# Kernel optimization log

Measured on AMD Instinct MI355X. Metric: run time of the kernel, lower is better.

Reference implementation:

```python
import jax, jax.numpy as jnp
import numpy as np

N = 100_000        # nodes
E_HALF = 1_600_000 # undirected edges; symmetrized -> 3.2M directed
N_IN, N_HEMB, N_HGCN, N_OUT = 128, 32, 32, 1


def setup_inputs() -> dict:
    key = jax.random.key(0)
    ks = jax.random.split(key, 8)
    x = jax.random.normal(ks[0], (N, N_IN), dtype=jnp.float32)
    t = jax.random.uniform(ks[1], (N,), dtype=jnp.float32)
    # symmetric edge list (A = A^T), matching the typical undirected-graph usage
    src = jax.random.randint(ks[2], (E_HALF,), 0, N)
    dst = jax.random.randint(ks[3], (E_HALF,), 0, N)
    row = jnp.concatenate([src, dst]).astype(jnp.int32)
    col = jnp.concatenate([dst, src]).astype(jnp.int32)
    s = 0.05
    W_emb = jax.random.normal(ks[4], (N_IN, N_HEMB), jnp.float32) * s
    b_emb = jnp.zeros((N_HEMB,), jnp.float32)
    W_gcn = jax.random.normal(ks[5], (N_HEMB, N_HGCN), jnp.float32) * s
    b_gcn = jnp.zeros((N_HGCN,), jnp.float32)
    W1 = jax.random.normal(ks[6], (N_HGCN + 2, N_HEMB), jnp.float32) * s
    b1 = jnp.zeros((N_HEMB,), jnp.float32)
    W2 = jax.random.normal(ks[7], (N_HEMB, N_OUT), jnp.float32) * s
    b2 = jnp.zeros((N_OUT,), jnp.float32)
    return dict(x=x, t=t, row=row, col=col,
                W_emb=W_emb, b_emb=b_emb, W_gcn=W_gcn, b_gcn=b_gcn,
                W1=W1, b1=b1, W2=W2, b2=b2)


def reference(x, t, row, col, W_emb, b_emb, W_gcn, b_gcn, W1, b1, W2, b2):
    n = x.shape[0]
    h = jax.nn.relu(x @ W_emb + b_emb)                        # [N, Hemb]
    # per-edge attention score via gather + dot
    att = jnp.einsum('eh,eh->e', h[row], h[col])              # [E]
    att = jnp.exp(att - att.max())                            # global-max stabilized exp
    # per-node softmax denominator (segment sum over neighbors) + eps
    deno = jax.ops.segment_sum(att, row, num_segments=n) + 1e-8
    att = att / deno[row]                                     # normalized edge attention
    # exposure z: attention-weighted neighbor treatments
    z = jax.ops.segment_sum(att * t[col], row, num_segments=n)  # [N]
    # GCNConv (unit edge values: set_value() is non-inplace so adj_t stays valueless;
    # PyG then fills 1s, adds self loops, symmetric D^-1/2 norm)
    deg = jax.ops.segment_sum(jnp.ones(row.shape, jnp.float32), col, num_segments=n) + 1.0
    dis = jax.lax.rsqrt(deg)                                  # [N], deg >= 1
    hw = h @ W_gcn                                            # [N, Hgcn]
    msg = dis[row][:, None] * hw[row]                         # [E, Hgcn]
    agg = jax.ops.segment_sum(msg, col, num_segments=n)       # [N, Hgcn]
    gcn = dis[:, None] * agg + (dis * dis)[:, None] * hw + b_gcn
    rep = h + jax.nn.relu(gcn)                                # residual node rep
    feats = jnp.concatenate([rep, t[:, None], z[:, None]], axis=1)  # [N, Hgcn+2]
    out = jax.nn.relu(feats @ W1 + b1) @ W2 + b2              # [N, 1]
    return out, rep, z
```

## Files before the change

### kernel.cpp

```cpp
#include <hip/hip_runtime.h>
#include <hip/hip_bf16.h>
#include <hip/hip_fp16.h>

static constexpr int HN = 32;
static constexpr int NIN = 128;
static constexpr int CH1 = 8192;
static constexpr int CAP2 = 12288;
static constexpr float SQRT_LOG2E = 1.2011224087864498f;

typedef _Float16 h2v __attribute__((ext_vector_type(2)));

__device__ __forceinline__ float bf2f(unsigned short u) {
    union { unsigned int i; float f; } v;
    v.i = ((unsigned int)u) << 16;
    return v.f;
}
__device__ __forceinline__ float ldf(const void* p, size_t i, int isbf) {
    return isbf ? bf2f(((const unsigned short*)p)[i]) : ((const float*)p)[i];
}
__device__ __forceinline__ unsigned int pack2h(float a, float b) {
    unsigned short ua = __half_as_ushort(__float2half_rn(a));
    unsigned short ub = __half_as_ushort(__float2half_rn(b));
    return (unsigned int)ua | ((unsigned int)ub << 16);
}
__device__ __forceinline__ float2 up2(unsigned int u) {
    __half2 h2;
    *reinterpret_cast<unsigned int*>(&h2) = u;
    return __half22float2(h2);
}
__device__ __forceinline__ float fd2(unsigned int a, unsigned int b, float c) {
#if __has_builtin(__builtin_amdgcn_fdot2)
    return __builtin_amdgcn_fdot2(__builtin_bit_cast(h2v, a),
                                  __builtin_bit_cast(h2v, b), c, false);
#else
    float2 fa = up2(a), fb = up2(b);
    return c + fa.x * fb.x + fa.y * fb.y;
#endif
}
__device__ __forceinline__ unsigned int fmap(float f) {
    unsigned int u = __float_as_uint(f);
    return (f >= 0.f) ? (u | 0x80000000u) : ~u;
}
__device__ __forceinline__ float funmap(unsigned int u) {
    return (u & 0x80000000u) ? __uint_as_float(u & 0x7FFFFFFFu)
                             : __uint_as_float(~u);
}

__global__ __launch_bounds__(256) void embed1_kernel(
    const void* __restrict__ x,
    const void* __restrict__ Wemb,
    const void* __restrict__ bemb,
    const int* __restrict__ flagp,
    float* __restrict__ h, int N)
{
    __shared__ float We[NIN * HN];
    __shared__ float be[HN];
    __shared__ float xs[32][NIN];
    const int tid = threadIdx.x;
    const int isbf = flagp[0];

    for (int i = tid; i < NIN * HN; i += 256) We[i] = ldf(Wemb, i, isbf);
    if (tid < HN) be[tid] = ldf(bemb, tid, isbf);

    const int n0 = blockIdx.x * 32;
    if (isbf) {
        const ushort4* x4 = (const ushort4*)((const unsigned short*)x + (size_t)n0 * NIN);
        for (int i = tid; i < 32 * (NIN / 4); i += 256) {
            ushort4 u = x4[i];
            int base = i * 4, n = base >> 7, k = base & (NIN - 1);
            xs[n][k] = bf2f(u.x); xs[n][k + 1] = bf2f(u.y);
            xs[n][k + 2] = bf2f(u.z); xs[n][k + 3] = bf2f(u.w);
        }
    } else {
        const float4* x4 = (const float4*)((const float*)x + (size_t)n0 * NIN);
        for (int i = tid; i < 32 * (NIN / 4); i += 256) {
            float4 u = x4[i];
            int base = i * 4, n = base >> 7, k = base & (NIN - 1);
            xs[n][k] = u.x; xs[n][k + 1] = u.y;
            xs[n][k + 2] = u.z; xs[n][k + 3] = u.w;
        }
    }
    __syncthreads();

    const int f = tid & 31, ns = tid >> 5;
    float a0 = be[f], a1 = be[f], a2 = be[f], a3 = be[f];
    #pragma unroll 8
    for (int k = 0; k < NIN; ++k) {
        float w = We[k * HN + f];
        a0 += xs[ns +  0][k] * w;
        a1 += xs[ns +  8][k] * w;
        a2 += xs[ns + 16][k] * w;
        a3 += xs[ns + 24][k] * w;
    }
    if (n0 + ns      < N) h[(size_t)(n0 + ns     ) * HN + f] = fmaxf(a0, 0.f);
    if (n0 + ns +  8 < N) h[(size_t)(n0 + ns +  8) * HN + f] = fmaxf(a1, 0.f);
    if (n0 + ns + 16 < N) h[(size_t)(n0 + ns + 16) * HN + f] = fmaxf(a2, 0.f);
    if (n0 + ns + 24 < N) h[(size_t)(n0 + ns + 24) * HN + f] = fmaxf(a3, 0.f);
}

__global__ __launch_bounds__(512) void bhist_kernel(
    const int* __restrict__ col, int* __restrict__ bucket_cnt, int E, int B,
    int* __restrict__ blkhist,
    const unsigned int* __restrict__ xw, int* __restrict__ flag)
{
    __shared__ int hist[512];
    const int t = threadIdx.x;
    const int e0 = blockIdx.x * CH1;
    for (int i = t; i < B; i += 512) hist[i] = 0;
    if (blockIdx.x == 0 && t < 64) {
        int hits = 0;
        #pragma unroll
        for (int k = 0; k < 2; ++k) {
            unsigned int w = xw[t + 64 * k];
            float a = bf2f((unsigned short)(w & 0xFFFFu));
            float aa = fabsf(a);
            if (a == 0.0f || (aa >= 0.000244140625f && aa <= 32.0f)) hits++;
        }
        #pragma unroll
        for (int m = 32; m; m >>= 1) hits += __shfl_xor(hits, m, 64);
        if (t == 0) flag[0] = (hits >= 64) ? 1 : 0;
    }
    __syncthreads();
    #pragma unroll
    for (int k = 0; k < CH1 / 512; ++k) {
        int e = e0 + k * 512 + t;
        if (e < E) atomicAdd(&hist[col[e] >> 8], 1);
    }
    __syncthreads();
    for (int i = t; i < B; i += 512) {
        int v = hist[i];
        blkhist[blockIdx.x * B + i] = v;
        if (v) atomicAdd(&bucket_cnt[i], v);
    }
}

__global__ __launch_bounds__(512) void bscan_kernel(
    const int* __restrict__ bucket_cnt, int* __restrict__ bucket_base,
    int* __restrict__ bucket_cursor, int* __restrict__ rowptr,
    int B, int N, int E)
{
    __shared__ int sc[512];
    __shared__ int orig[512];
    const int t = threadIdx.x;
    int v0 = (t < B) ? bucket_cnt[t] : 0;
    sc[t] = v0; orig[t] = v0;
    __syncthreads();
    for (int o = 1; o < 512; o <<= 1) {
        int v = (t >= o) ? sc[t - o] : 0;
        __syncthreads();
        sc[t] += v;
        __syncthreads();
    }
    if (t < B) {
        int ex = sc[t] - orig[t];
        bucket_base[t] = ex;
        bucket_cursor[t] = ex;
    }
    if (t == 0) { bucket_base[B] = E; rowptr[N] = E; }
}

__global__ __launch_bounds__(512) void phase1_kernel(
    const int* __restrict__ row, const int* __restrict__ col,
    const int* __restrict__ blkhist,
    int* __restrict__ bucket_cursor, int* __restrict__ bucketed, int E, int B)
{
    __shared__ int hist[512];
    __shared__ int sc[512];
    __shared__ int cnt[512];
    __shared__ int gbase[512];
    __shared__ int word[CH1];
    __shared__ int dst[CH1];
    const int t = threadIdx.x;
    const int e0 = blockIdx.x * CH1;
    const int M = (E - e0 < CH1) ? (E - e0) : CH1;

    for (int i = t; i < B; i += 512) {
        hist[i] = blkhist[blockIdx.x * B + i];
        cnt[i] = 0;
    }
    __syncthreads();
    sc[t] = (t < B) ? hist[t] : 0;
    __syncthreads();
    for (int o = 1; o < 512; o <<= 1) {
        int v = (t >= o) ? sc[t - o] : 0;
        __syncthreads();
        sc[t] += v;
        __syncthreads();
    }
    if (t < B && hist[t])
        gbase[t] = atomicAdd(&bucket_cursor[t], hist[t]);
    __syncthreads();
    #pragma unroll
    for (int k = 0; k < CH1 / 512; ++k) {
        int e = e0 + k * 512 + t;
        if (e < E) {
            int c = col[e], r = row[e];
            int b = c >> 8;
            int lr = atomicAdd(&cnt[b], 1);
            int p = sc[b] - hist[b] + lr;
            word[p] = (r << 8) | (c & 255);
            dst[p] = gbase[b] + lr;
        }
    }
    __syncthreads();
    for (int i = t; i < M; i += 512)
        bucketed[dst[i]] = word[i];
}

__global__ __launch_bounds__(256) void phase2_kernel(
    const int* __restrict__ bucketed, const int* __restrict__ bucket_base,
    int* __restrict__ rowptr, int* __restrict__ csr_src, int N)
{
    __shared__ int stage[CAP2];
    __shared__ unsigned short rank_s[CAP2];
    __shared__ int cnt[256];
    __shared__ int sc[256];
    __shared__ int loc[256];
    const int t = threadIdx.x, b = blockIdx.x;
    const int node0 = b << 8;
    const int s0 = bucket_base[b], s1 = bucket_base[b + 1];
    const int segsz = s1 - s0;
    cnt[t] = 0;
    __syncthreads();
    for (int i = s0 + t; i < s1; i += 256) {
        int lc = bucketed[i] & 255;
        int r = atomicAdd(&cnt[lc], 1);
        if (i - s0 < CAP2) rank_s[i - s0] = (unsigned short)r;
    }
    __syncthreads();
    int c = cnt[t];
    sc[t] = c;
    __syncthreads();
    for (int o = 1; o < 256; o <<= 1) {
        int v = (t >= o) ? sc[t - o] : 0;
        __syncthreads();
        sc[t] += v;
        __syncthreads();
    }
    int ex = sc[t] - c;
    loc[t] = ex;
    if (node0 + t < N) rowptr[node0 + t] = s0 + ex;
    cnt[t] = 0;
    __syncthreads();
    if (segsz <= CAP2) {
        for (int i = s0 + t; i < s1; i += 256) {
            int w = bucketed[i];
            stage[loc[w & 255] + rank_s[i - s0]] = w >> 8;
        }
        __syncthreads();
        for (int i = t; i < segsz; i += 256) csr_src[s0 + i] = stage[i];
    } else {
        for (int i = s0 + t; i < s1; i += 256) {
            int w = bucketed[i];
            int lc = w & 255;
            int off = loc[lc] + atomicAdd(&cnt[lc], 1);
            csr_src[s0 + off] = w >> 8;
        }
    }
}

__global__ __launch_bounds__(256) void embed2_kernel(
    const float* __restrict__ h, const void* __restrict__ Wgcn,
    const int* __restrict__ rowptr, const int* __restrict__ flagp,
    uint4* __restrict__ packed, int N)
{
    __shared__ float Wg[HN * HN];
    __shared__ float hs[32][HN + 1];
    __shared__ float ws[32][HN + 1];
    const int tid = threadIdx.x;
    const int isbf = flagp[0];
    for (int i = tid; i < HN * HN; i += 256) Wg[i] = ldf(Wgcn, i, isbf);
    const int n0 = blockIdx.x * 32;
    for (int i = tid; i < 32 * HN; i += 256) {
        int n = i >> 5, f = i & 31;
        hs[n][f] = (n0 + n < N) ? h[(size_t)(n0 + n) * HN + f] : 0.f;
    }
    __syncthreads();
    const int f = tid & 31, ns = tid >> 5;
    #pragma unroll
    for (int g = 0; g < 4; ++g) {
        int n = ns + 8 * g, v = n0 + n;
        float acc = 0.f;
        #pragma unroll
        for (int k = 0; k < HN; ++k) acc += hs[n][k] * Wg[k * HN + f];
        float dis = (v < N) ? rsqrtf((float)(rowptr[v + 1] - rowptr[v]) + 1.0f) : 0.f;
        ws[n][f] = dis * acc;
    }
    __syncthreads();
    const int n = tid >> 3, jj = tid & 7, v = n0 + n;
    if (v < N) {
        uint4 w;
        w.x = pack2h(hs[n][4 * jj + 0] * SQRT_LOG2E, hs[n][4 * jj + 1] * SQRT_LOG2E);
        w.y = pack2h(hs[n][4 * jj + 2] * SQRT_LOG2E, hs[n][4 * jj + 3] * SQRT_LOG2E);
        w.z = pack2h(ws[n][4 * jj + 0], ws[n][4 * jj + 1]);
        w.w = pack2h(ws[n][4 * jj + 2], ws[n][4 * jj + 3]);
        packed[(size_t)v * 8 + jj] = w;
    }
}

__global__ __launch_bounds__(256) void passB_kernel(
    const float* __restrict__ h, const uint4* __restrict__ packed,
    const int* __restrict__ csr_src, const int* __restrict__ rowptr,
    const void* __restrict__ t, const void* __restrict__ bgcn,
    const int* __restrict__ flagp,
    float* __restrict__ outr, float* __restrict__ outz,
    float* __restrict__ out0_ml, float* __restrict__ denout, int N)
{
    const int tid = threadIdx.x;
    const int lane = tid & 31;
    const int sub = lane >> 3;
    const int j = lane & 7;
    const int v = blockIdx.x * 8 + (tid >> 5);
    if (v >= N) return;
    const int isbf = flagp[0];

    const float4* h4 = (const float4*)h;
    float4 hv = h4[(size_t)v * 8 + j];
    uint4 sw = packed[(size_t)v * 8 + j];
    float2 wsv0 = up2(sw.z), wsv1 = up2(sw.w);
    const int s = rowptr[v], e2 = rowptr[v + 1];

    float m = -1e30f, den = 0.f, num = 0.f;
    float ax = 0.f, ay = 0.f, az = 0.f, aw = 0.f;
    int i = s + sub;
    for (; i + 12 < e2; i += 16) {
        int r0 = csr_src[i];
        int r1 = csr_src[i + 4];
        int r2 = csr_src[i + 8];
        int r3 = csr_src[i + 12];
        uint4 w0 = packed[(size_t)r0 * 8 + j];
        uint4 w1 = packed[(size_t)r1 * 8 + j];
        uint4 w2 = packed[(size_t)r2 * 8 + j];
        uint4 w3 = packed[(size_t)r3 * 8 + j];
        float tr0 = ldf(t, r0, isbf);
        float tr1 = ldf(t, r1, isbf);
        float tr2 = ldf(t, r2, isbf);
        float tr3 = ldf(t, r3, isbf);
        float p0 = fd2(w0.x, sw.x, fd2(w0.y, sw.y, 0.f));
        float p1 = fd2(w1.x, sw.x, fd2(w1.y, sw.y, 0.f));
        float p2 = fd2(w2.x, sw.x, fd2(w2.y, sw.y, 0.f));
        float p3 = fd2(w3.x, sw.x, fd2(w3.y, sw.y, 0.f));
        p0 += __shfl_xor(p0, 1, 32);
        p0 += __shfl_xor(p0, 2, 32);
        p0 += __shfl_xor(p0, 4, 32);
        p1 += __shfl_xor(p1, 1, 32);
        p1 += __shfl_xor(p1, 2, 32);
        p1 += __shfl_xor(p1, 4, 32);
        p2 += __shfl_xor(p2, 1, 32);
        p2 += __shfl_xor(p2, 2, 32);
        p2 += __shfl_xor(p2, 4, 32);
        p3 += __shfl_xor(p3, 1, 32);
        p3 += __shfl_xor(p3, 2, 32);
        p3 += __shfl_xor(p3, 4, 32);
        float2 a00 = up2(w0.z), a01 = up2(w0.w);
        float2 a10 = up2(w1.z), a11 = up2(w1.w);
        float2 a20 = up2(w2.z), a21 = up2(w2.w);
        float2 a30 = up2(w3.z), a31 = up2(w3.w);
        ax += (a00.x + a10.x) + (a20.x + a30.x);
        ay += (a00.y + a10.y) + (a20.y + a30.y);
        az += (a01.x + a11.x) + (a21.x + a31.x);
        aw += (a01.y + a11.y) + (a21.y + a31.y);
        float mn = fmaxf(m, fmaxf(fmaxf(p0, p1), fmaxf(p2, p3)));
        float corr = exp2f(m - mn);
        float e0 = exp2f(p0 - mn), e1 = exp2f(p1 - mn);
        float e2x = exp2f(p2 - mn), e3 = exp2f(p3 - mn);
        den = den * corr + (e0 + e1) + (e2x + e3);
        num = num * corr + (e0 * tr0 + e1 * tr1) + (e2x * tr2 + e3 * tr3);
        m = mn;
    }
    for (; i + 4 < e2; i += 8) {
        int r0 = csr_src[i];
        int r1 = csr_src[i + 4];
        uint4 w0 = packed[(size_t)r0 * 8 + j];
        uint4 w1 = packed[(size_t)r1 * 8 + j];
        float tr0 = ldf(t, r0, isbf);
        float tr1 = ldf(t, r1, isbf);
        float p0 = fd2(w0.x, sw.x, fd2(w0.y, sw.y, 0.f));
        float p1 = fd2(w1.x, sw.x, fd2(w1.y, sw.y, 0.f));
        p0 += __shfl_xor(p0, 1, 32);
        p0 += __shfl_xor(p0, 2, 32);
        p0 += __shfl_xor(p0, 4, 32);
        p1 += __shfl_xor(p1, 1, 32);
        p1 += __shfl_xor(p1, 2, 32);
        p1 += __shfl_xor(p1, 4, 32);
        float2 a00 = up2(w0.z), a01 = up2(w0.w);
        float2 a10 = up2(w1.z), a11 = up2(w1.w);
        ax += a00.x + a10.x; ay += a00.y + a10.y;
        az += a01.x + a11.x; aw += a01.y + a11.y;
        float mn = fmaxf(m, fmaxf(p0, p1));
        float corr = exp2f(m - mn);
        float e0 = exp2f(p0 - mn), e1 = exp2f(p1 - mn);
        den = den * corr + e0 + e1;
        num = num * corr + e0 * tr0 + e1 * tr1;
        m = mn;
    }
    if (i < e2) {
        int r0 = csr_src[i];
        uint4 w0 = packed[(size_t)r0 * 8 + j];
        float tr0 = ldf(t, r0, isbf);
        float p0 = fd2(w0.x, sw.x, fd2(w0.y, sw.y, 0.f));
        p0 += __shfl_xor(p0, 1, 32);
        p0 += __shfl_xor(p0, 2, 32);
        p0 += __shfl_xor(p0, 4, 32);
        float2 a00 = up2(w0.z), a01 = up2(w0.w);
        ax += a00.x; ay += a00.y; az += a01.x; aw += a01.y;
        float mn = fmaxf(m, p0);
        float corr = exp2f(m - mn);
        float e0 = exp2f(p0 - mn);
        den = den * corr + e0;
        num = num * corr + e0 * tr0;
        m = mn;
    }
    #pragma unroll
    for (int o = 8; o <= 16; o <<= 1) {
        float mo = __shfl_xor(m, o, 32);
        float dno = __shfl_xor(den, o, 32);
        float nmo = __shfl_xor(num, o, 32);
        float mn = fmaxf(m, mo);
        float ca = exp2f(m - mn), cb = exp2f(mo - mn);
        den = den * ca + dno * cb;
        num = num * ca + nmo * cb;
        m = mn;
        ax += __shfl_xor(ax, o, 32);
        ay += __shfl_xor(ay, o, 32);
        az += __shfl_xor(az, o, 32);
        aw += __shfl_xor(aw, o, 32);
    }

    float dv = rsqrtf((float)(e2 - s) + 1.0f);
    float4 rep;
    rep.x = hv.x + fmaxf(dv * (ax + wsv0.x) + ldf(bgcn, 4 * j + 0, isbf), 0.f);
    rep.y = hv.y + fmaxf(dv * (ay + wsv0.y) + ldf(bgcn, 4 * j + 1, isbf), 0.f);
    rep.z = hv.z + fmaxf(dv * (az + wsv1.x) + ldf(bgcn, 4 * j + 2, isbf), 0.f);
    rep.w = hv.w + fmaxf(dv * (aw + wsv1.y) + ldf(bgcn, 4 * j + 3, isbf), 0.f);
    if (sub == 0)
        ((float4*)outr)[(size_t)v * 8 + j] = rep;
    if (lane == 0) {
        outz[v]    = num / fmaxf(den, 1e-37f);
        out0_ml[v] = m;
        denout[v]  = den;
    }
}

__global__ __launch_bounds__(256) void amax1_kernel(
    const float* __restrict__ ml, unsigned int* __restrict__ amax_u, int N)
{
    float m = -INFINITY;
    for (int i = blockIdx.x * 256 + threadIdx.x; i < N; i += 256 * 256)
        m = fmaxf(m, ml[i]);
    #pragma unroll
    for (int s = 32; s; s >>= 1) m = fmaxf(m, __shfl_xor(m, s, 64));
    __shared__ float sm[4];
    if ((threadIdx.x & 63) == 0) sm[threadIdx.x >> 6] = m;
    __syncthreads();
    if (threadIdx.x == 0) {
        float bm = fmaxf(fmaxf(sm[0], sm[1]), fmaxf(sm[2], sm[3]));
        atomicMax(amax_u, fmap(bm));
    }
}

__global__ __launch_bounds__(256) void final_kernel(
    const float* __restrict__ rep_in,
    const void* __restrict__ t, const int* __restrict__ flagp,
    const unsigned int* __restrict__ amax_u, const float* __restrict__ denarr,
    const void* __restrict__ W1, const void* __restrict__ b1,
    const void* __restrict__ W2, const void* __restrict__ b2,
    float* __restrict__ out0, float* __restrict__ outz, int N)
{
    __shared__ float W1s[34 * HN];
    __shared__ float b1s[HN], W2s[HN];
    __shared__ float b2s;
    const int tid = threadIdx.x;
    const int isbf = flagp[0];
    for (int i = tid; i < 34 * HN; i += 256) W1s[i] = ldf(W1, i, isbf);
    if (tid < HN) {
        b1s[tid] = ldf(b1, tid, isbf);
        W2s[tid] = ldf(W2, tid, isbf);
    }
    if (tid == 0) b2s = ldf(b2, 0, isbf);
    __syncthreads();

    const int lane = tid & 31;
    const int v = blockIdx.x * 8 + (tid >> 5);
    if (v >= N) return;

    float rep = rep_in[(size_t)v * HN + lane];
    float ml  = out0[v];
    float den = denarr[v];
    float zh  = outz[v];
    float am  = funmap(amax_u[0]);
    float term = (1e-8f / den) * exp2f(am - ml);
    float z = zh / (1.0f + term);
    float tv = ldf(t, v, isbf);

    float acc = b1s[lane] + tv * W1s[32 * HN + lane] + z * W1s[33 * HN + lane];
    #pragma unroll
    for (int k = 0; k < HN; ++k)
        acc += __shfl(rep, k, 32) * W1s[k * HN + lane];
    float f1 = fmaxf(acc, 0.f);
    float o = f1 * W2s[lane];
    #pragma unroll
    for (int m = 16; m; m >>= 1) o += __shfl_xor(o, m, 32);

    if (lane == 0) {
        out0[v] = o + b2s;
        outz[v] = z;
    }
}

extern "C" void kernel_launch(void* const* d_in, const int* in_sizes, int n_in,
                              void* d_out, int out_size, void* d_ws, size_t ws_size,
                              hipStream_t stream)
{
    const int N = out_size / 34;
    const int E = in_sizes[2];

    const void* x    = d_in[0];
    const void* t    = d_in[1];
    const int* row   = (const int*)d_in[2];
    const int* col   = (const int*)d_in[3];
    const void* Wemb = d_in[4];
    const void* bemb = d_in[5];
    const void* Wgcn = d_in[6];
    const void* bgcn = d_in[7];
    const void* W1   = d_in[8];
    const void* b1   = d_in[9];
    const void* W2   = d_in[10];
    const void* b2   = d_in[11];

    const int B   = (N + 255) >> 8;
    const int NB1 = (E + CH1 - 1) / CH1;

    char* wsb = (char*)d_ws;
    size_t off = 0;
    float* h        = (float*)(wsb + off); off += (size_t)N * HN * 4;
    size_t hwbytes  = (size_t)N * HN * 4;
    if ((size_t)E * 4 > hwbytes) hwbytes = (size_t)E * 4;
    char*  hwreg    = wsb + off;           off += hwbytes;
    int*   csr_src  = (int*)(wsb + off);   off += (size_t)E * 4;
    int*   rowptr   = (int*)(wsb + off);   off += (size_t)(N + 1) * 4;
    float* den      = (float*)(wsb + off); off += (size_t)N * 4;
    int*   bucket_cnt    = (int*)(wsb + off); off += (size_t)B * 4;
    unsigned int* amax_u = (unsigned int*)(wsb + off); off += 4;
    int*   bucket_base   = (int*)(wsb + off); off += (size_t)(B + 1) * 4;
    int*   bucket_cursor = (int*)(wsb + off); off += (size_t)B * 4;
    int*   flag     = (int*)(wsb + off);   off += 4;

    int*   bucketed = (int*)hwreg;
    uint4* packed   = (uint4*)hwreg;
    int*   blkhist  = csr_src;

    hipMemsetAsync(bucket_cnt, 0, (size_t)(B + 1) * 4, stream);

    bhist_kernel<<<NB1, 512, 0, stream>>>(col, bucket_cnt, E, B, blkhist,
                                          (const unsigned int*)x, flag);
    embed1_kernel<<<(N + 31) / 32, 256, 0, stream>>>(x, Wemb, bemb, flag, h, N);
    bscan_kernel<<<1, 512, 0, stream>>>(bucket_cnt, bucket_base,
                                        bucket_cursor, rowptr, B, N, E);
    phase1_kernel<<<NB1, 512, 0, stream>>>(row, col, blkhist, bucket_cursor,
                                           bucketed, E, B);
    phase2_kernel<<<B, 256, 0, stream>>>(bucketed, bucket_base, rowptr,
                                         csr_src, N);
    embed2_kernel<<<(N + 31) / 32, 256, 0, stream>>>(h, Wgcn, rowptr, flag,
                                                     packed, N);

    float* outp = (float*)d_out;
    float* out0 = outp;
    float* outr = outp + N;
    float* outz = outp + (size_t)N * 33;

    passB_kernel<<<(N + 7) / 8, 256, 0, stream>>>(
        h, packed, csr_src, rowptr, t, bgcn, flag, outr, outz, out0, den, N);
    amax1_kernel<<<256, 256, 0, stream>>>(out0, amax_u, N);
    final_kernel<<<(N + 7) / 8, 256, 0, stream>>>(
        outr, t, flag, amax_u, den, W1, b1, W2, b2, out0, outz, N);
}
```

Baseline: 335.1 us.

## Rewrite embedding GEMV to stream x rows through registers with wave shuffles

```diff
diff --git a/kernel.cpp b/kernel.cpp
--- a/kernel.cpp
+++ b/kernel.cpp
@@ -27,6 +27,12 @@
     __half2 h2;
     *reinterpret_cast<unsigned int*>(&h2) = u;
     return __half22float2(h2);
+}
+__device__ __forceinline__ float2 upbf2(unsigned int u) {
+    float2 r;
+    r.x = bf2f((unsigned short)(u & 0xFFFFu));
+    r.y = bf2f((unsigned short)(u >> 16));
+    return r;
 }
 __device__ __forceinline__ float fd2(unsigned int a, unsigned int b, float c) {
 #if __has_builtin(__builtin_amdgcn_fdot2)
@@ -53,49 +59,80 @@
     const int* __restrict__ flagp,
     float* __restrict__ h, int N)
 {
-    __shared__ float We[NIN * HN];
+    __shared__ float2 Ws2[64 * 32];
     __shared__ float be[HN];
-    __shared__ float xs[32][NIN];
     const int tid = threadIdx.x;
     const int isbf = flagp[0];
 
-    for (int i = tid; i < NIN * HN; i += 256) We[i] = ldf(Wemb, i, isbf);
+    for (int i = tid; i < NIN * HN; i += 256) {
+        int k = i >> 5, f = i & 31;
+        float v = ldf(Wemb, i, isbf);
+        ((float*)Ws2)[(((k >> 1) * 32 + f) << 1) | (k & 1)] = v;
+    }
     if (tid < HN) be[tid] = ldf(bemb, tid, isbf);
-
-    const int n0 = blockIdx.x * 32;
-    if (isbf) {
-        const ushort4* x4 = (const ushort4*)((const unsigned short*)x + (size_t)n0 * NIN);
-        for (int i = tid; i < 32 * (NIN / 4); i += 256) {
-            ushort4 u = x4[i];
-            int base = i * 4, n = base >> 7, k = base & (NIN - 1);
-            xs[n][k] = bf2f(u.x); xs[n][k + 1] = bf2f(u.y);
-            xs[n][k + 2] = bf2f(u.z); xs[n][k + 3] = bf2f(u.w);
+    __syncthreads();
+
+    const int f = tid & 31;
+    const int s = tid >> 5;
+    const int n0 = blockIdx.x * 64;
+
+    #pragma unroll
+    for (int it = 0; it < 4; ++it) {
+        int na = n0 + it * 16 + s;
+        int nb = na + 8;
+        int nac = (na < N) ? na : 0;
+        int nbc = (nb < N) ? nb : 0;
+        float acca = be[f], accb = be[f];
+        if (isbf) {
+            const unsigned int* x2 = (const unsigned int*)x;
+            unsigned int a0 = x2[(size_t)nac * 64 + f];
+            unsigned int a1 = x2[(size_t)nac * 64 + 32 + f];
+            unsigned int b0 = x2[(size_t)nbc * 64 + f];
+            unsigned int b1 = x2[(size_t)nbc * 64 + 32 + f];
+            #pragma unroll
+            for (int kk = 0; kk < 32; ++kk) {
+                float2 w2 = Ws2[(kk << 5) | f];
+                float2 va = upbf2(__shfl(a0, kk, 32));
+                float2 vb = upbf2(__shfl(b0, kk, 32));
+                acca += va.x * w2.x + va.y * w2.y;
+                accb += vb.x * w2.x + vb.y * w2.y;
+            }
+            #pragma unroll
+            for (int kk = 0; kk < 32; ++kk) {
+                float2 w2 = Ws2[((kk + 32) << 5) | f];
+                float2 va = upbf2(__shfl(a1, kk, 32));
+                float2 vb = upbf2(__shfl(b1, kk, 32));
+                acca += va.x * w2.x + va.y * w2.y;
+                accb += vb.x * w2.x + vb.y * w2.y;
+            }
+        } else {
+            const float2* x2 = (const float2*)x;
+            float2 a0 = x2[(size_t)nac * 64 + f];
+            float2 a1 = x2[(size_t)nac * 64 + 32 + f];
+            float2 b0 = x2[(size_t)nbc * 64 + f];
+            float2 b1 = x2[(size_t)nbc * 64 + 32 + f];
+            #pragma unroll
+            for (int kk = 0; kk < 32; ++kk) {
+                float2 w2 = Ws2[(kk << 5) | f];
+                float2 va, vb;
+                va.x = __shfl(a0.x, kk, 32); va.y = __shfl(a0.y, kk, 32);
+                vb.x = __shfl(b0.x, kk, 32); vb.y = __shfl(b0.y, kk, 32);
+                acca += va.x * w2.x + va.y * w2.y;
+                accb += vb.x * w2.x + vb.y * w2.y;
+            }
+            #pragma unroll
+            for (int kk = 0; kk < 32; ++kk) {
+                float2 w2 = Ws2[((kk + 32) << 5) | f];
+                float2 va, vb;
+                va.x = __shfl(a1.x, kk, 32); va.y = __shfl(a1.y, kk, 32);
+                vb.x = __shfl(b1.x, kk, 32); vb.y = __shfl(b1.y, kk, 32);
+                acca += va.x * w2.x + va.y * w2.y;
+                accb += vb.x * w2.x + vb.y * w2.y;
+            }
         }
-    } else {
-        const float4* x4 = (const float4*)((const float*)x + (size_t)n0 * NIN);
-        for (int i = tid; i < 32 * (NIN / 4); i += 256) {
-            float4 u = x4[i];
-            int base = i * 4, n = base >> 7, k = base & (NIN - 1);
-            xs[n][k] = u.x; xs[n][k + 1] = u.y;
-            xs[n][k + 2] = u.z; xs[n][k + 3] = u.w;
-        }
-    }
-    __syncthreads();
-
-    const int f = tid & 31, ns = tid >> 5;
-    float a0 = be[f], a1 = be[f], a2 = be[f], a3 = be[f];
-    #pragma unroll 8
-    for (int k = 0; k < NIN; ++k) {
-        float w = We[k * HN + f];
-        a0 += xs[ns +  0][k] * w;
-        a1 += xs[ns +  8][k] * w;
-        a2 += xs[ns + 16][k] * w;
-        a3 += xs[ns + 24][k] * w;
-    }
-    if (n0 + ns      < N) h[(size_t)(n0 + ns     ) * HN + f] = fmaxf(a0, 0.f);
-    if (n0 + ns +  8 < N) h[(size_t)(n0 + ns +  8) * HN + f] = fmaxf(a1, 0.f);
-    if (n0 + ns + 16 < N) h[(size_t)(n0 + ns + 16) * HN + f] = fmaxf(a2, 0.f);
-    if (n0 + ns + 24 < N) h[(size_t)(n0 + ns + 24) * HN + f] = fmaxf(a3, 0.f);
+        if (na < N) h[(size_t)na * HN + f] = fmaxf(acca, 0.f);
+        if (nb < N) h[(size_t)nb * HN + f] = fmaxf(accb, 0.f);
+    }
 }
 
 __global__ __launch_bounds__(512) void bhist_kernel(
@@ -129,7 +166,7 @@
     __syncthreads();
     for (int i = t; i < B; i += 512) {
         int v = hist[i];
-        blkhist[blockIdx.x * B + i] = v;
+        blkhist[(size_t)blockIdx.x * B + i] = v;
         if (v) atomicAdd(&bucket_cnt[i], v);
     }
 }
@@ -175,7 +212,7 @@
     const int M = (E - e0 < CH1) ? (E - e0) : CH1;
 
     for (int i = t; i < B; i += 512) {
-        hist[i] = blkhist[blockIdx.x * B + i];
+        hist[i] = blkhist[(size_t)blockIdx.x * B + i];
         cnt[i] = 0;
     }
     __syncthreads();
@@ -554,7 +591,7 @@
 
     bhist_kernel<<<NB1, 512, 0, stream>>>(col, bucket_cnt, E, B, blkhist,
                                           (const unsigned int*)x, flag);
-    embed1_kernel<<<(N + 31) / 32, 256, 0, stream>>>(x, Wemb, bemb, flag, h, N);
+    embed1_kernel<<<(N + 63) / 64, 256, 0, stream>>>(x, Wemb, bemb, flag, h, N);
     bscan_kernel<<<1, 512, 0, stream>>>(bucket_cnt, bucket_base,
                                         bucket_cursor, rowptr, B, N, E);
     phase1_kernel<<<NB1, 512, 0, stream>>>(row, col, blkhist, bucket_cursor,
```

Result: slower. 394.3 us (+17.6%).
